# Kernel optimization log

Measured on AMD Instinct MI355X. Metric: run time of the kernel, lower is better.

Reference implementation:

```python
import jax, jax.numpy as jnp
import numpy as np

B, S, D, H = 4, 2048, 1024, 16
HD = D // H  # head_dim = 64


def setup_inputs() -> dict:
    key = jax.random.key(0)
    k1, k2, k3 = jax.random.split(key, 3)
    x = jax.random.normal(k1, (B, S, D), dtype=jnp.float32)
    W_attn = jax.random.normal(k2, (D, 3 * D), dtype=jnp.float32) * (1.0 / np.sqrt(D))
    b_attn = jnp.zeros((3 * D,), dtype=jnp.float32)
    W_proj = jax.random.normal(k3, (D, D), dtype=jnp.float32) * (1.0 / np.sqrt(D))
    b_proj = jnp.zeros((D,), dtype=jnp.float32)
    return {"x": x, "W_attn": W_attn, "b_attn": b_attn, "W_proj": W_proj, "b_proj": b_proj}


def reference(x, W_attn, b_attn, W_proj, b_proj):
    bsz, seq_len, d = x.shape
    n_head = H
    head_dim = d // n_head
    qkv = x @ W_attn + b_attn                      # [B,S,3D]
    q, k, v = jnp.split(qkv, 3, axis=-1)           # each [B,S,D]
    # -> [B,H,S,hd]
    q = q.reshape(bsz, seq_len, n_head, head_dim).transpose(0, 2, 1, 3)
    k = k.reshape(bsz, seq_len, n_head, head_dim).transpose(0, 2, 1, 3)
    v = v.reshape(bsz, seq_len, n_head, head_dim).transpose(0, 2, 1, 3)
    scale = 1.0 / np.sqrt(head_dim).astype(np.float32)
    att = jnp.einsum("bhqd,bhkd->bhqk", q, k) * scale  # [B,H,S,S]
    causal = jnp.tril(jnp.ones((seq_len, seq_len), dtype=bool))
    att = jnp.where(causal[None, None], att, jnp.float32(-jnp.inf))
    att = jax.nn.softmax(att, axis=-1)
    y = jnp.einsum("bhqk,bhkd->bhqd", att, v)       # [B,H,S,hd]
    y = y.transpose(0, 2, 1, 3).reshape(bsz, seq_len, d)
    return y @ W_proj + b_proj
```

## Files before the change

### kernel.cpp

```cpp
#include <hip/hip_runtime.h>

typedef __attribute__((ext_vector_type(8))) short short8;
typedef __attribute__((ext_vector_type(8))) __bf16 bf16x8;
typedef __attribute__((ext_vector_type(2))) __bf16 bf16x2;
typedef __attribute__((ext_vector_type(4))) float f32x4;
typedef __attribute__((ext_vector_type(2))) unsigned int uint2v;

#define LOG2E 1.44269504088896340736f

__device__ __forceinline__ unsigned short f2b(float f) {
  unsigned u = __builtin_bit_cast(unsigned, f);
  u += 0x7fffu + ((u >> 16) & 1u);
  return (unsigned short)(u >> 16);
}
__device__ __forceinline__ float b2f(unsigned short s) {
  unsigned u = (unsigned)s << 16;
  return __builtin_bit_cast(float, u);
}
__device__ __forceinline__ bf16x8 asbf(short8 s) { return __builtin_bit_cast(bf16x8, s); }

__device__ __forceinline__ void gl_lds16(const void* g, void* l) {
  __builtin_amdgcn_global_load_lds(
      (const __attribute__((address_space(1))) void*)g,
      (__attribute__((address_space(3))) void*)l, 16, 0, 0);
}

__device__ __forceinline__ unsigned lds_a(const void* p) {
  return (unsigned)(size_t)(__attribute__((address_space(3))) const void*)p;
}

__device__ __forceinline__ unsigned pk_bf16(float a, float b) {
  bf16x2 v;
  v[0] = (__bf16)a;
  v[1] = (__bf16)b;
  return __builtin_bit_cast(unsigned, v);
}

__global__ void k_cvt_bf16(const float* __restrict__ x, unsigned short* __restrict__ o, int n) {
  int i = (blockIdx.x * 256 + threadIdx.x) * 4;
  if (i >= n) return;
  float4 v = *(const float4*)(x + i);
  ushort4 r;
  r.x = f2b(v.x); r.y = f2b(v.y); r.z = f2b(v.z); r.w = f2b(v.w);
  *(ushort4*)(o + i) = r;
}

__global__ void k_transpose_bf16(const float* __restrict__ W, unsigned short* __restrict__ Wt,
                                 int R, int C) {
  __shared__ float tile[64][65];
  const int tc = blockIdx.x, tr = blockIdx.y;
  const int r0 = tr * 64, c0 = tc * 64;
  for (int it = 0; it < 16; ++it) {
    int lin = it * 256 + threadIdx.x;
    int r = lin >> 6, c = lin & 63;
    tile[r][c] = W[(size_t)(r0 + r) * C + c0 + c];
  }
  __syncthreads();
  for (int it = 0; it < 16; ++it) {
    int lin = it * 256 + threadIdx.x;
    int orr = lin >> 6, oc = lin & 63;
    Wt[(size_t)(c0 + orr) * R + r0 + oc] = f2b(tile[oc][orr]);
  }
}

template <bool OUT_BF16>
__global__ __launch_bounds__(256)
void k_gemm_bt(const unsigned short* __restrict__ A, const unsigned short* __restrict__ Bt,
               const float* __restrict__ bias, void* __restrict__ Cp,
               int M, int N, int K) {
  __shared__ unsigned short As[128 * 32];
  __shared__ unsigned short Bs[128 * 32];
  const int tid = threadIdx.x;
  const int lane = tid & 63, w = tid >> 6;
  const int g = lane >> 4, l15 = lane & 15;
  const int ntn = N >> 7;
  const int nwg = gridDim.x;
  const int bid = blockIdx.x;
  const int cpx = nwg >> 3;
  const int swz = (bid & 7) * cpx + (bid >> 3);
  const int tm = swz / ntn, tn = swz % ntn;
  const int wr = w >> 1, wc = w & 1;

  f32x4 acc[4][4] = {};

  const int j0 = tid;
  const int j1 = 256 + tid;
  const int r0s = j0 >> 2, c0s = ((j0 & 3) ^ (r0s & 3)) * 8;
  const int r1s = j1 >> 2, c1s = ((j1 & 3) ^ (r1s & 3)) * 8;
  const unsigned short* Abase = A + (size_t)(tm * 128) * K;
  const unsigned short* Bbase = Bt + (size_t)(tn * 128) * K;

  const int KS = K >> 5;
  for (int kt = 0; kt < KS; ++kt) {
    const int k0 = kt << 5;
    __syncthreads();
    gl_lds16(Abase + (size_t)r0s * K + k0 + c0s, (char*)As + j0 * 16);
    gl_lds16(Abase + (size_t)r1s * K + k0 + c1s, (char*)As + j1 * 16);
    gl_lds16(Bbase + (size_t)r0s * K + k0 + c0s, (char*)Bs + j0 * 16);
    gl_lds16(Bbase + (size_t)r1s * K + k0 + c1s, (char*)Bs + j1 * 16);
    __syncthreads();
    short8 af[4], bfr[4];
    for (int m = 0; m < 4; ++m) {
      int row = wr * 64 + m * 16 + l15;
      int ch = g ^ (row & 3);
      af[m] = *(const short8*)((const char*)As + row * 64 + ch * 16);
    }
    for (int n = 0; n < 4; ++n) {
      int row = wc * 64 + n * 16 + l15;
      int ch = g ^ (row & 3);
      bfr[n] = *(const short8*)((const char*)Bs + row * 64 + ch * 16);
    }
    for (int m = 0; m < 4; ++m)
      for (int n = 0; n < 4; ++n)
        acc[m][n] =
            __builtin_amdgcn_mfma_f32_16x16x32_bf16(asbf(af[m]), asbf(bfr[n]), acc[m][n], 0, 0, 0);
  }

  const int crow0 = tm * 128 + wr * 64 + g * 4;
  const int ccol0 = tn * 128 + wc * 64 + l15;
  for (int n = 0; n < 4; ++n) {
    int col = ccol0 + n * 16;
    float bv = bias[col];
    for (int m = 0; m < 4; ++m)
      for (int j = 0; j < 4; ++j) {
        int row = crow0 + m * 16 + j;
        float v = acc[m][n][j] + bv;
        if (OUT_BF16)
          ((unsigned short*)Cp)[(size_t)row * N + col] = f2b(v);
        else
          ((float*)Cp)[(size_t)row * N + col] = v;
      }
  }
}

template <int KVH>
__device__ __forceinline__ void pv_step(unsigned vaddr, const char* pbase,
                                        int l15, int g, f32x4* o, f32x4& ol,
                                        short8 onesb) {
  int poff = (l15 * 128 + KVH * 64 + g * 16) ^ ((l15 & 7) << 4);
  short8 pa = *(const short8*)(pbase + poff);
  uint2v t0[4], t1[4];
#pragma unroll
  for (int n = 0; n < 4; ++n) {
    asm volatile("ds_read_b64_tr_b16 %0, %1 offset:%2"
                 : "=v"(t0[n]) : "v"(vaddr), "i"(n * 2048 + KVH * 1024));
    asm volatile("ds_read_b64_tr_b16 %0, %1 offset:%2"
                 : "=v"(t1[n]) : "v"(vaddr), "i"(n * 2048 + KVH * 1024 + 512));
  }
  asm volatile("s_waitcnt lgkmcnt(0)" ::: "memory");
  __builtin_amdgcn_sched_barrier(0);
  __builtin_amdgcn_s_setprio(1);
#pragma unroll
  for (int n = 0; n < 4; ++n) {
    union { uint2v u[2]; short8 s; } uu;
    uu.u[0] = t0[n]; uu.u[1] = t1[n];
    o[n] = __builtin_amdgcn_mfma_f32_16x16x32_bf16(asbf(pa), asbf(uu.s), o[n], 0, 0, 0);
  }
  ol = __builtin_amdgcn_mfma_f32_16x16x32_bf16(asbf(pa), asbf(onesb), ol, 0, 0, 0);
  __builtin_amdgcn_s_setprio(0);
}

__global__ __launch_bounds__(256)
void k_attn(const unsigned short* __restrict__ qkv, unsigned short* __restrict__ y) {
  constexpr int SEQ = 2048, TD = 3072, DM = 1024, NT = 32;
  __shared__ unsigned short Kl[2][4096];
  __shared__ unsigned short Vl[2][4096];
  __shared__ unsigned short Pl[4][1024];

  const int f = blockIdx.y * 16 + blockIdx.x;
  const int wrk = (f & 7) * 128 + (f >> 3);
  const int bh = wrk >> 4, pr = wrk & 15;
  const int b = bh >> 4, h = bh & 15;
  const int tid = threadIdx.x;
  const int lane = tid & 63, w = tid >> 6;
  const int g = lane >> 4, l15 = lane & 15;

  const size_t base = (size_t)b * SEQ * TD + h * 64;
  const unsigned short* Kg0 = qkv + base + 1024;
  const unsigned short* Vg0 = qkv + base + 2048;

  short8 onesb;
#pragma unroll
  for (int i = 0; i < 8; ++i) onesb[i] = (short)0x3F80;

  auto stage = [&](int buf, int c) {
    const unsigned short* Kg = Kg0 + (size_t)(c * 64) * TD;
    const unsigned short* Vg = Vg0 + (size_t)(c * 64) * TD;
#pragma unroll
    for (int t = 0; t < 2; ++t) {
      int j = t * 256 + tid;
      int r = j >> 3, cc = j & 7;
      int cck = cc ^ (r & 7);
      gl_lds16(Kg + (size_t)r * TD + cck * 8, (char*)Kl[buf] + j * 16);
      int kv = ((j >> 1) & 3) | (((j >> 5) & 1) << 2) | (((j >> 3) & 3) << 3) |
               (((j >> 6) & 1) << 5);
      int d0 = ((j >> 7) << 4) | ((j & 1) << 3);
      gl_lds16(Vg + (size_t)kv * TD + d0, (char*)Vl[buf] + j * 16);
    }
  };

  for (int half = 0; half < 2; ++half) {
    const int qt = half ? (NT - 1 - pr) : pr;
    const int q0 = qt * 64;

    short8 qf[2];
    {
      const unsigned short* qrow = qkv + base + (size_t)(q0 + w * 16 + l15) * TD;
#pragma unroll
      for (int kh = 0; kh < 2; ++kh) {
        short8 t = *(const short8*)(qrow + kh * 32 + g * 8);
#pragma unroll
        for (int i = 0; i < 8; ++i)
          t[i] = (short)f2b(b2f((unsigned short)t[i]) * (0.125f * LOG2E));
        qf[kh] = t;
      }
    }

    f32x4 o[4] = {};
    f32x4 ol = {};

    const int nch = qt + 1;
    int cur = 0;
    stage(0, 0);
    for (int c = 0; c < nch; ++c) {
      if (c + 1 < nch) {
        stage(cur ^ 1, c + 1);
        asm volatile("s_waitcnt vmcnt(4)" ::: "memory");
      } else {
        asm volatile("s_waitcnt vmcnt(0)" ::: "memory");
      }
      __builtin_amdgcn_s_barrier();

      f32x4 sv[4];
      __builtin_amdgcn_s_setprio(1);
#pragma unroll
      for (int ff = 0; ff < 4; ++ff) {
        f32x4 s = {};
        int kv = ff * 16 + l15;
#pragma unroll
        for (int kh = 0; kh < 2; ++kh) {
          int ch = (kh * 4 + g) ^ (kv & 7);
          short8 kf = *(const short8*)((const char*)Kl[cur] + kv * 128 + ch * 16);
          s = __builtin_amdgcn_mfma_f32_16x16x32_bf16(asbf(kf), asbf(qf[kh]), s, 0, 0, 0);
        }
        sv[ff] = s;
      }
      __builtin_amdgcn_s_setprio(0);
      if (c == qt) {
#pragma unroll
        for (int ff = 0; ff < 4; ++ff)
#pragma unroll
          for (int r = 0; r < 4; ++r)
            if (ff * 16 + g * 4 + r > w * 16 + l15) sv[ff][r] = -128.f;
      }

#pragma unroll
      for (int ff = 0; ff < 4; ++ff) {
        float p0 = __builtin_amdgcn_exp2f(sv[ff][0]);
        float p1 = __builtin_amdgcn_exp2f(sv[ff][1]);
        float p2 = __builtin_amdgcn_exp2f(sv[ff][2]);
        float p3 = __builtin_amdgcn_exp2f(sv[ff][3]);
        unsigned w0 = pk_bf16(p0, p1);
        unsigned w1 = pk_bf16(p2, p3);
        unsigned long long pk = (unsigned long long)w0 | ((unsigned long long)w1 << 32);
        int off = (l15 * 128 + ff * 32 + g * 8) ^ ((l15 & 7) << 4);
        *(unsigned long long*)((char*)Pl[w] + off) = pk;
      }

      const unsigned vaddr = lds_a((const char*)Vl[cur] + g * 128 + l15 * 8);
      const char* pbase = (const char*)Pl[w];
      pv_step<0>(vaddr, pbase, l15, g, o, ol, onesb);
      pv_step<1>(vaddr, pbase, l15, g, o, ol, onesb);

      __builtin_amdgcn_s_barrier();
      cur ^= 1;
    }

    float lj[4];
#pragma unroll
    for (int j = 0; j < 4; ++j) lj[j] = 1.f / ol[j];
#pragma unroll
    for (int n = 0; n < 4; ++n)
#pragma unroll
      for (int j = 0; j < 4; ++j) {
        int row = q0 + w * 16 + g * 4 + j;
        int col = h * 64 + n * 16 + l15;
        y[(size_t)(b * SEQ + row) * DM + col] = f2b(o[n][j] * lj[j]);
      }
  }
}

extern "C" void kernel_launch(void* const* d_in, const int* in_sizes, int n_in,
                              void* d_out, int out_size, void* d_ws, size_t ws_size,
                              hipStream_t stream) {
  const float* x = (const float*)d_in[0];
  const float* W_attn = (const float*)d_in[1];
  const float* b_attn = (const float*)d_in[2];
  const float* W_proj = (const float*)d_in[3];
  const float* b_proj = (const float*)d_in[4];
  float* out = (float*)d_out;

  const int B = 4, S = 2048, D = 1024;
  const int M = B * S;
  const int TD = 3 * D;

  char* ws = (char*)d_ws;
  unsigned short* qkvb = (unsigned short*)ws;
  unsigned short* xb = (unsigned short*)(ws + (size_t)M * TD * 2);
  unsigned short* Wat = (unsigned short*)(ws + (size_t)M * TD * 2 + (size_t)M * D * 2);
  unsigned short* Wpt = Wat + (size_t)TD * D;

  k_cvt_bf16<<<(M * D) / 1024, 256, 0, stream>>>(x, xb, M * D);
  k_transpose_bf16<<<dim3(TD / 64, D / 64), 256, 0, stream>>>(W_attn, Wat, D, TD);
  k_transpose_bf16<<<dim3(D / 64, D / 64), 256, 0, stream>>>(W_proj, Wpt, D, D);

  k_gemm_bt<true><<<(M / 128) * (TD / 128), 256, 0, stream>>>(xb, Wat, b_attn, qkvb, M, TD, D);
  k_attn<<<dim3(16, 64), 256, 0, stream>>>(qkvb, xb);
  k_gemm_bt<false><<<(M / 128) * (D / 128), 256, 0, stream>>>(xb, Wpt, b_proj, out, M, D, D);
}
```

Before: 178.1 us.

## Replace GEMM with 256-row tiled, double-buffered, 8-wave pipelined MFMA kernel

Replaces the 128x128 single-buffered GEMM with a 512-thread kernel using 256xBN tiles, a K-step of 64 and two LDS buffers. Global-to-LDS loads for the next tiles are interleaved with MFMA work per quarter, gated by explicit vmcnt waits and barriers, with setprio raised around the MFMA block. The aim is to hide load latency and raise arithmetic intensity for both the QKV and output projections. In exchange it needs more LDS and registers and depends on hand-tuned waitcnt values being correct.

```diff
diff --git a/kernel.cpp b/kernel.cpp
--- a/kernel.cpp
+++ b/kernel.cpp
@@ -63,69 +63,143 @@
   }
 }
 
-template <bool OUT_BF16>
-__global__ __launch_bounds__(256)
-void k_gemm_bt(const unsigned short* __restrict__ A, const unsigned short* __restrict__ Bt,
+template <int BNW, bool OUT_BF16>
+__global__ __launch_bounds__(512)
+void k_gemm256(const unsigned short* __restrict__ A, const unsigned short* __restrict__ Bt,
                const float* __restrict__ bias, void* __restrict__ Cp,
                int M, int N, int K) {
-  __shared__ unsigned short As[128 * 32];
-  __shared__ unsigned short Bs[128 * 32];
+  constexpr int BN = BNW * 4;
+  constexpr int NR = BNW / 16;
+  __shared__ unsigned short lds[2][(256 + BN) * 64];
+
   const int tid = threadIdx.x;
-  const int lane = tid & 63, w = tid >> 6;
+  const int wv = tid >> 6, lane = tid & 63;
   const int g = lane >> 4, l15 = lane & 15;
-  const int ntn = N >> 7;
+  const int wr = wv >> 2, wc = wv & 3;
+
+  const int ntn = N / BN;
   const int nwg = gridDim.x;
   const int bid = blockIdx.x;
   const int cpx = nwg >> 3;
   const int swz = (bid & 7) * cpx + (bid >> 3);
   const int tm = swz / ntn, tn = swz % ntn;
-  const int wr = w >> 1, wc = w & 1;
-
-  f32x4 acc[4][4] = {};
-
-  const int j0 = tid;
-  const int j1 = 256 + tid;
-  const int r0s = j0 >> 2, c0s = ((j0 & 3) ^ (r0s & 3)) * 8;
-  const int r1s = j1 >> 2, c1s = ((j1 & 3) ^ (r1s & 3)) * 8;
-  const unsigned short* Abase = A + (size_t)(tm * 128) * K;
-  const unsigned short* Bbase = Bt + (size_t)(tn * 128) * K;
-
-  const int KS = K >> 5;
-  for (int kt = 0; kt < KS; ++kt) {
-    const int k0 = kt << 5;
-    __syncthreads();
-    gl_lds16(Abase + (size_t)r0s * K + k0 + c0s, (char*)As + j0 * 16);
-    gl_lds16(Abase + (size_t)r1s * K + k0 + c1s, (char*)As + j1 * 16);
-    gl_lds16(Bbase + (size_t)r0s * K + k0 + c0s, (char*)Bs + j0 * 16);
-    gl_lds16(Bbase + (size_t)r1s * K + k0 + c1s, (char*)Bs + j1 * 16);
-    __syncthreads();
-    short8 af[4], bfr[4];
-    for (int m = 0; m < 4; ++m) {
-      int row = wr * 64 + m * 16 + l15;
-      int ch = g ^ (row & 3);
-      af[m] = *(const short8*)((const char*)As + row * 64 + ch * 16);
-    }
-    for (int n = 0; n < 4; ++n) {
-      int row = wc * 64 + n * 16 + l15;
-      int ch = g ^ (row & 3);
-      bfr[n] = *(const short8*)((const char*)Bs + row * 64 + ch * 16);
-    }
-    for (int m = 0; m < 4; ++m)
-      for (int n = 0; n < 4; ++n)
-        acc[m][n] =
-            __builtin_amdgcn_mfma_f32_16x16x32_bf16(asbf(af[m]), asbf(bfr[n]), acc[m][n], 0, 0, 0);
-  }
-
-  const int crow0 = tm * 128 + wr * 64 + g * 4;
-  const int ccol0 = tn * 128 + wc * 64 + l15;
-  for (int n = 0; n < 4; ++n) {
+
+  const unsigned short* Ab = A + (size_t)(tm * 256) * K;
+  const unsigned short* Bb = Bt + (size_t)(tn * BN) * K;
+
+  const int NT = K >> 6, NI = NT >> 1;
+
+  auto As = [&](int buf) -> char* { return (char*)&lds[buf][0]; };
+  auto Bs = [&](int buf) -> char* { return (char*)&lds[buf][256 * 64]; };
+
+  auto stageB = [&](int buf, int t) {
+#pragma unroll
+    for (int it = 0; it < NR; ++it) {
+      int cidx = it * 8 + wv;
+      int row = cidx * 8 + (lane >> 3);
+      int sc = (lane & 7) ^ (row & 7);
+      gl_lds16(Bb + (size_t)row * K + t * 64 + sc * 8, Bs(buf) + cidx * 1024 + lane * 16);
+    }
+  };
+  auto stageA = [&](int buf, int t, int q) {
+    int row0 = (wv < 4) ? (q * 32 + wv * 8) : (128 + q * 32 + (wv - 4) * 8);
+    int row = row0 + (lane >> 3);
+    int sc = (lane & 7) ^ (row & 7);
+    gl_lds16(Ab + (size_t)row * K + t * 64 + sc * 8, As(buf) + row0 * 128 + lane * 16);
+  };
+
+  auto rdA = [&](int buf, int q, int ms, int kh) -> short8 {
+    int row = wr * 128 + q * 32 + ms * 16 + l15;
+    int ch = (kh * 4 + g) ^ (row & 7);
+    return *(const short8*)(As(buf) + row * 128 + ch * 16);
+  };
+  auto rdB = [&](int buf, int n, int kh) -> short8 {
+    int row = wc * BNW + n * 16 + l15;
+    int ch = (kh * 4 + g) ^ (row & 7);
+    return *(const short8*)(Bs(buf) + row * 128 + ch * 16);
+  };
+
+  f32x4 acc[8][NR] = {};
+  short8 bfr[NR][2];
+
+  stageB(0, 0);
+#pragma unroll
+  for (int q = 0; q < 4; ++q) stageA(0, 0, q);
+  stageB(1, 1);
+#pragma unroll
+  for (int q = 0; q < 3; ++q) stageA(1, 1, q);
+  if constexpr (NR == 4) asm volatile("s_waitcnt vmcnt(7)" ::: "memory");
+  else                   asm volatile("s_waitcnt vmcnt(5)" ::: "memory");
+  __builtin_amdgcn_s_barrier();
+
+  for (int i = 0; i < NI; ++i) {
+    const int t0 = 2 * i;
+#pragma unroll
+    for (int half = 0; half < 2; ++half) {
+#pragma unroll
+      for (int q = 0; q < 4; ++q) {
+        short8 afr[2][2];
+#pragma unroll
+        for (int ms = 0; ms < 2; ++ms)
+#pragma unroll
+          for (int kh = 0; kh < 2; ++kh) afr[ms][kh] = rdA(half, q, ms, kh);
+        if (q == 0) {
+#pragma unroll
+          for (int n = 0; n < NR; ++n)
+#pragma unroll
+            for (int kh = 0; kh < 2; ++kh) bfr[n][kh] = rdB(half, n, kh);
+        }
+        if (half == 0) {
+          if (q == 0) stageA(1, t0 + 1, 3);
+          if (q == 1 && t0 + 2 < NT) { stageB(0, t0 + 2); stageA(0, t0 + 2, 0); }
+          if (q == 2 && t0 + 2 < NT) stageA(0, t0 + 2, 1);
+          if (q == 3 && t0 + 2 < NT) stageA(0, t0 + 2, 2);
+        } else {
+          if (q == 0 && t0 + 2 < NT) stageA(0, t0 + 2, 3);
+          if (q == 1 && t0 + 3 < NT) stageB(1, t0 + 3);
+          if (q == 2 && t0 + 3 < NT) stageA(1, t0 + 3, 0);
+          if (q == 3 && t0 + 3 < NT) { stageA(1, t0 + 3, 1); stageA(1, t0 + 3, 2); }
+        }
+        __builtin_amdgcn_s_barrier();
+        asm volatile("s_waitcnt lgkmcnt(0)" ::: "memory");
+        __builtin_amdgcn_sched_barrier(0);
+        __builtin_amdgcn_s_setprio(1);
+#pragma unroll
+        for (int n = 0; n < NR; ++n)
+#pragma unroll
+          for (int ms = 0; ms < 2; ++ms)
+#pragma unroll
+            for (int kh = 0; kh < 2; ++kh)
+              acc[q * 2 + ms][n] = __builtin_amdgcn_mfma_f32_16x16x32_bf16(
+                  asbf(afr[ms][kh]), asbf(bfr[n][kh]), acc[q * 2 + ms][n], 0, 0, 0);
+        __builtin_amdgcn_s_setprio(0);
+        if (q == 3) {
+          const bool more = (half == 0) ? (t0 + 2 < NT) : (t0 + 3 < NT);
+          if (more) {
+            if constexpr (NR == 4) asm volatile("s_waitcnt vmcnt(7)" ::: "memory");
+            else                   asm volatile("s_waitcnt vmcnt(5)" ::: "memory");
+          } else {
+            asm volatile("s_waitcnt vmcnt(0)" ::: "memory");
+          }
+        }
+        __builtin_amdgcn_s_barrier();
+      }
+    }
+  }
+
+  const int crow0 = tm * 256 + wr * 128 + g * 4;
+  const int ccol0 = tn * BN + wc * BNW + l15;
+#pragma unroll
+  for (int n = 0; n < NR; ++n) {
     int col = ccol0 + n * 16;
     float bv = bias[col];
-    for (int m = 0; m < 4; ++m)
+#pragma unroll
+    for (int mq = 0; mq < 8; ++mq)
+#pragma unroll
       for (int j = 0; j < 4; ++j) {
-        int row = crow0 + m * 16 + j;
-        float v = acc[m][n][j] + bv;
-        if (OUT_BF16)
+        int row = crow0 + mq * 16 + j;
+        float v = acc[mq][n][j] + bv;
+        if constexpr (OUT_BF16)
           ((unsigned short*)Cp)[(size_t)row * N + col] = f2b(v);
         else
           ((float*)Cp)[(size_t)row * N + col] = v;
@@ -314,7 +388,7 @@
   k_transpose_bf16<<<dim3(TD / 64, D / 64), 256, 0, stream>>>(W_attn, Wat, D, TD);
   k_transpose_bf16<<<dim3(D / 64, D / 64), 256, 0, stream>>>(W_proj, Wpt, D, D);
 
-  k_gemm_bt<true><<<(M / 128) * (TD / 128), 256, 0, stream>>>(xb, Wat, b_attn, qkvb, M, TD, D);
+  k_gemm256<64, true><<<(M / 256) * (TD / 256), 512, 0, stream>>>(xb, Wat, b_attn, qkvb, M, TD, D);
   k_attn<<<dim3(16, 64), 256, 0, stream>>>(qkvb, xb);
-  k_gemm_bt<false><<<(M / 128) * (D / 128), 256, 0, stream>>>(xb, Wpt, b_proj, out, M, D, D);
-}
+  k_gemm256<32, false><<<(M / 256) * (D / 128), 512, 0, stream>>>(xb, Wpt, b_proj, out, M, D, D);
+}
```

After: 175.5 us. Within noise of the previous version (-1.4%).
